# Kernel optimization log

Hardware: AMD Instinct MI355X
Metric: run time of the kernel (lower is better)

The kernel has to match this reference:

```python
import jax, jax.numpy as jnp
import numpy as np

E = 1024
H = 16
HD = E // H


def setup_inputs() -> dict:
    key = jax.random.key(0)
    k1, k2, k3, k4, k5 = jax.random.split(key, 5)
    x = jax.random.normal(k1, (2, 2048, E), dtype=jnp.float32)
    s = 1.0 / np.sqrt(E)
    qkv_w = jax.random.uniform(k2, (3 * E, E), jnp.float32, -s, s)
    qkv_b = jax.random.uniform(k3, (3 * E,), jnp.float32, -s, s)
    o_w = jax.random.uniform(k4, (E, E), jnp.float32, -s, s)
    o_b = jax.random.uniform(k5, (E,), jnp.float32, -s, s)
    return {"x": x, "qkv_w": qkv_w, "qkv_b": qkv_b, "o_w": o_w, "o_b": o_b}


def reference(x, qkv_w, qkv_b, o_w, o_b):
    B, T, _ = x.shape
    # qkv projection (torch Linear: x @ W.T + b)
    qkv = x @ qkv_w.T + qkv_b  # [B,T,3E]
    q, k, v = jnp.split(qkv, 3, axis=-1)
    # [B,H,T,HD]
    q = q.reshape(B, T, H, HD).transpose(0, 2, 1, 3)
    k = k.reshape(B, T, H, HD).transpose(0, 2, 1, 3)
    v = v.reshape(B, T, H, HD).transpose(0, 2, 1, 3)
    scores = jnp.einsum('bhqd,bhkd->bhqk', q, k) / np.sqrt(HD)
    causal = jnp.tril(jnp.ones((T, T), dtype=bool))
    scores = jnp.where(causal, scores, -jnp.inf)
    attn = jax.nn.softmax(scores, axis=-1)  # dropout disabled (eval mode)
    y = jnp.einsum('bhqk,bhkd->bhqd', attn, v)
    y = y.transpose(0, 2, 1, 3).reshape(B, T, E)
    return y @ o_w.T + o_b
```

## Files before the change

kernel.cpp:

```cpp
#include <hip/hip_runtime.h>
#include <hip/hip_bf16.h>
#include <math.h>

#define BATCH 2
#define SEQ   2048
#define EMB   1024
#define NH    16
#define HD    64
#define M_ROWS (BATCH * SEQ)

typedef __attribute__((ext_vector_type(8))) short bf16x8;
typedef __attribute__((ext_vector_type(4))) float f32x4;

__device__ __forceinline__ ushort f2bf(float f) {
    unsigned u = __float_as_uint(f);
    unsigned lsb = (u >> 16) & 1u;
    u += 0x7fffu + lsb;
    return (ushort)(u >> 16);
}

__device__ __forceinline__ unsigned cvt_pk_bf16(float lo, float hi) {
    unsigned r;
    asm("v_cvt_pk_bf16_f32 %0, %1, %2" : "=v"(r) : "v"(lo), "v"(hi));
    return r;
}

__device__ __forceinline__ void gload_lds16(const void* g, void* l) {
    __builtin_amdgcn_global_load_lds(
        (const __attribute__((address_space(1))) unsigned int*)g,
        (__attribute__((address_space(3))) unsigned int*)l, 16, 0, 0);
}

__global__ __launch_bounds__(256) void cvt3_f32_bf16(
    const float* __restrict__ s1, const float* __restrict__ s2,
    const float* __restrict__ s3, ushort* __restrict__ out,
    int n1, int n2)
{
    int i = (blockIdx.x * 256 + threadIdx.x) * 4;
    const float* src;
    int off;
    if (i < n1)            { src = s1; off = i; }
    else if (i < n1 + n2)  { src = s2; off = i - n1; }
    else                   { src = s3; off = i - n1 - n2; }
    float4 v = *reinterpret_cast<const float4*>(&src[off]);
    uint2 pk;
    pk.x = cvt_pk_bf16(v.x, v.y);
    pk.y = cvt_pk_bf16(v.z, v.w);
    *reinterpret_cast<uint2*>(&out[i]) = pk;
}

template <int MODE>
__global__ __launch_bounds__(256) void gemm_mfma_abt(
    const ushort* __restrict__ A, const ushort* __restrict__ B,
    const float* __restrict__ bias, float* __restrict__ Cout,
    ushort* __restrict__ qkb, ushort* __restrict__ vtb,
    int M, int N, int K)
{
    __shared__ ushort Al[128 * 64];
    __shared__ ushort Bl[128 * 64];

    const int tid  = threadIdx.x;
    const int lane = tid & 63;
    const int wave = tid >> 6;
    const int wr   = wave >> 1;
    const int wc   = wave & 1;
    const int l15  = lane & 15;
    const int l4   = lane >> 4;
    const int m0   = blockIdx.y * 128;
    const int n0   = blockIdx.x * 128;

    f32x4 acc[4][4];
#pragma unroll
    for (int m = 0; m < 4; ++m)
#pragma unroll
        for (int n = 0; n < 4; ++n)
#pragma unroll
            for (int r = 0; r < 4; ++r) acc[m][n][r] = 0.f;

    for (int k0 = 0; k0 < K; k0 += 64) {
#pragma unroll
        for (int it = 0; it < 4; ++it) {
            int chunk = tid + it * 256;
            int row = chunk >> 3;
            int kc  = (chunk & 7) * 8;
            gload_lds16(&A[(size_t)(m0 + row) * K + k0 + kc], &Al[chunk * 8]);
            gload_lds16(&B[(size_t)(n0 + row) * K + k0 + kc], &Bl[chunk * 8]);
        }
        __syncthreads();

#pragma unroll
        for (int kk = 0; kk < 2; ++kk) {
            const int ko = kk * 32 + l4 * 8;
            bf16x8 a[4], b[4];
#pragma unroll
            for (int m = 0; m < 4; ++m)
                a[m] = *reinterpret_cast<const bf16x8*>(
                    &Al[(wr * 64 + m * 16 + l15) * 64 + ko]);
#pragma unroll
            for (int n = 0; n < 4; ++n)
                b[n] = *reinterpret_cast<const bf16x8*>(
                    &Bl[(wc * 64 + n * 16 + l15) * 64 + ko]);
            __builtin_amdgcn_s_setprio(1);
#pragma unroll
            for (int m = 0; m < 4; ++m)
#pragma unroll
                for (int n = 0; n < 4; ++n)
                    acc[m][n] = __builtin_amdgcn_mfma_f32_16x16x32_bf16(
                        a[m], b[n], acc[m][n], 0, 0, 0);
            __builtin_amdgcn_s_setprio(0);
        }
        __syncthreads();
    }

#pragma unroll
    for (int n = 0; n < 4; ++n) {
        const int col = n0 + wc * 64 + n * 16 + l15;
        const float bv = bias[col];
        if (MODE == 0) {
#pragma unroll
            for (int m = 0; m < 4; ++m) {
                const int row0 = m0 + wr * 64 + m * 16 + l4 * 4;
#pragma unroll
                for (int r = 0; r < 4; ++r)
                    Cout[(size_t)(row0 + r) * N + col] = acc[m][n][r] + bv;
            }
        } else if (col < 2 * EMB) {
#pragma unroll
            for (int m = 0; m < 4; ++m) {
                const int row0 = m0 + wr * 64 + m * 16 + l4 * 4;
#pragma unroll
                for (int r = 0; r < 4; ++r)
                    qkb[(size_t)(row0 + r) * 2048 + col] = f2bf(acc[m][n][r] + bv);
            }
        } else {
            const int h = (col - 2 * EMB) >> 6;
            const int d = col & 63;
#pragma unroll
            for (int m = 0; m < 4; ++m) {
                const int row0 = m0 + wr * 64 + m * 16 + l4 * 4;
                const int bb = row0 >> 11;
                const int t  = row0 & 2047;
                uint2 pk;
                pk.x = cvt_pk_bf16(acc[m][n][0] + bv, acc[m][n][1] + bv);
                pk.y = cvt_pk_bf16(acc[m][n][2] + bv, acc[m][n][3] + bv);
                *reinterpret_cast<uint2*>(
                    &vtb[((size_t)(bb * 16 + h) * 64 + d) * 2048 + t]) = pk;
            }
        }
    }
}

__global__ __launch_bounds__(512) void attn_mfma(
    const ushort* __restrict__ qk, const ushort* __restrict__ vt,
    ushort* __restrict__ y)
{
    __shared__ alignas(16) ushort Kl[4][4096];
    __shared__ alignas(16) ushort Vl[4][4096];
    __shared__ alignas(16) ushort QP[8192];

    const int tid  = threadIdx.x;
    const int lane = tid & 63;
    const int w    = tid >> 6;
    const int l15  = lane & 15;
    const int l4   = lane >> 4;

    const int id  = blockIdx.x;
    const int xcd = id & 7;
    const int bh  = xcd * 4 + ((id >> 3) & 3);
    const int pp  = id >> 5;
    const int b   = bh >> 4;
    const int h   = bh & 15;

    const ushort* qbase = qk + (size_t)b * SEQ * 2048 + h * HD;
    const ushort* kbase = qbase + EMB;
    const ushort* vbase = vt + (size_t)bh * HD * SEQ;

    const int swz   = (l15 & 7) << 4;
    const int koff0 = ((l4 * 16) ^ swz) >> 1;
    const int koff1 = ((64 + l4 * 16) ^ swz) >> 1;

    int pso[4];
#pragma unroll
    for (int n = 0; n < 4; ++n) pso[n] = ((n * 32 + l4 * 8) ^ swz) >> 1;

    const short OBF = (short)0x3F80;
    const bf16x8 ones = {OBF, OBF, OBF, OBF, OBF, OBF, OBF, OBF};
    const float BETA = 0.18033688f;

    const int qrow = (w * 16 + l15) * 64;

    const int sr = tid >> 3;
    const int sc = ((tid & 7) ^ (sr & 7)) << 3;
    const int i2 = tid + 512;
    const int qr2 = i2 >> 3;
    const int qc2 = ((i2 & 7) ^ (qr2 & 7)) << 3;

#pragma unroll
    for (int pass = 0; pass < 2; ++pass) {
        const int qt  = pass ? (15 - pp) : pp;
        const int nkv = 2 * qt + 2;

        gload_lds16(qbase + (size_t)(qt * 128 + sr) * 2048 + sc, &QP[tid * 8]);
        gload_lds16(qbase + (size_t)(qt * 128 + qr2) * 2048 + qc2, &QP[i2 * 8]);
        gload_lds16(kbase + (size_t)sr * 2048 + sc, &Kl[0][tid * 8]);
        gload_lds16(kbase + (size_t)(64 + sr) * 2048 + sc, &Kl[1][tid * 8]);
        gload_lds16(vbase + (size_t)sr * 2048 + sc, &Vl[0][tid * 8]);
        gload_lds16(vbase + (size_t)sr * 2048 + 64 + sc, &Vl[1][tid * 8]);
        __syncthreads();

        const bf16x8 qf0 = *reinterpret_cast<const bf16x8*>(&QP[qrow + koff0]);
        const bf16x8 qf1 = *reinterpret_cast<const bf16x8*>(&QP[qrow + koff1]);

        f32x4 o[4];
#pragma unroll
        for (int n = 0; n < 4; ++n)
#pragma unroll
            for (int r = 0; r < 4; ++r) o[n][r] = 0.f;
        f32x4 lacc = {0.f, 0.f, 0.f, 0.f};
        float m = -3.0e38f;

        auto computeTile = [&](const ushort* Kb, const ushort* Vb, int kkt) {
            bf16x8 kf[4][2];
#pragma unroll
            for (int n = 0; n < 4; ++n) {
                kf[n][0] = *reinterpret_cast<const bf16x8*>(
                    &Kb[(n * 16 + l15) * 64 + koff0]);
                kf[n][1] = *reinterpret_cast<const bf16x8*>(
                    &Kb[(n * 16 + l15) * 64 + koff1]);
            }
            f32x4 s[4];
            __builtin_amdgcn_s_setprio(1);
#pragma unroll
            for (int n = 0; n < 4; ++n) {
                f32x4 z = {0.f, 0.f, 0.f, 0.f};
                z = __builtin_amdgcn_mfma_f32_16x16x32_bf16(kf[n][0], qf0, z, 0, 0, 0);
                s[n] = __builtin_amdgcn_mfma_f32_16x16x32_bf16(kf[n][1], qf1, z, 0, 0, 0);
            }
            __builtin_amdgcn_s_setprio(0);

            bf16x8 vf[4][2];
#pragma unroll
            for (int n = 0; n < 4; ++n) {
                vf[n][0] = *reinterpret_cast<const bf16x8*>(
                    &Vb[(n * 16 + l15) * 64 + koff0]);
                vf[n][1] = *reinterpret_cast<const bf16x8*>(
                    &Vb[(n * 16 + l15) * 64 + koff1]);
            }

            if (kkt >= nkv - 2) {
                const int q0 = qt * 128 + w * 16 + l15;
#pragma unroll
                for (int n = 0; n < 4; ++n)
#pragma unroll
                    for (int r = 0; r < 4; ++r) {
                        int kg = kkt * 64 + n * 16 + l4 * 4 + r;
                        if (kg > q0) s[n][r] = -3.0e38f;
                    }
            }

            float a0 = fmaxf(fmaxf(s[0][0], s[0][1]), fmaxf(s[0][2], s[0][3]));
            float a1 = fmaxf(fmaxf(s[1][0], s[1][1]), fmaxf(s[1][2], s[1][3]));
            float a2 = fmaxf(fmaxf(s[2][0], s[2][1]), fmaxf(s[2][2], s[2][3]));
            float a3 = fmaxf(fmaxf(s[3][0], s[3][1]), fmaxf(s[3][2], s[3][3]));
            float pm = fmaxf(fmaxf(a0, a1), fmaxf(a2, a3)) * BETA;

            if (__any(pm > m + 8.0f)) {
                float tm = fmaxf(pm, __shfl_xor(pm, 16));
                tm = fmaxf(tm, __shfl_xor(tm, 32));
                float mn = fmaxf(m, tm);
                float al = exp2f(m - mn);
                m = mn;
                float b0 = __shfl(al, l4 * 4 + 0, 16);
                float b1 = __shfl(al, l4 * 4 + 1, 16);
                float b2 = __shfl(al, l4 * 4 + 2, 16);
                float b3 = __shfl(al, l4 * 4 + 3, 16);
                lacc[0] *= b0; lacc[1] *= b1; lacc[2] *= b2; lacc[3] *= b3;
#pragma unroll
                for (int n = 0; n < 4; ++n) {
                    o[n][0] *= b0; o[n][1] *= b1; o[n][2] *= b2; o[n][3] *= b3;
                }
            }

#pragma unroll
            for (int n = 0; n < 4; ++n) {
                float pa = exp2f(fmaf(s[n][0], BETA, -m));
                float pb = exp2f(fmaf(s[n][1], BETA, -m));
                float pc = exp2f(fmaf(s[n][2], BETA, -m));
                float pd = exp2f(fmaf(s[n][3], BETA, -m));
                uint2 pk;
                pk.x = cvt_pk_bf16(pa, pb);
                pk.y = cvt_pk_bf16(pc, pd);
                *reinterpret_cast<uint2*>(&QP[qrow + pso[n]]) = pk;
            }

            bf16x8 pf0 = *reinterpret_cast<const bf16x8*>(&QP[qrow + koff0]);
            bf16x8 pf1 = *reinterpret_cast<const bf16x8*>(&QP[qrow + koff1]);
            __builtin_amdgcn_s_setprio(1);
            lacc = __builtin_amdgcn_mfma_f32_16x16x32_bf16(pf0, ones, lacc, 0, 0, 0);
            lacc = __builtin_amdgcn_mfma_f32_16x16x32_bf16(pf1, ones, lacc, 0, 0, 0);
#pragma unroll
            for (int n = 0; n < 4; ++n) {
                o[n] = __builtin_amdgcn_mfma_f32_16x16x32_bf16(pf0, vf[n][0], o[n], 0, 0, 0);
                o[n] = __builtin_amdgcn_mfma_f32_16x16x32_bf16(pf1, vf[n][1], o[n], 0, 0, 0);
            }
            __builtin_amdgcn_s_setprio(0);
        };

        for (int kk = 0; kk < nkv; kk += 2) {
            if (kk + 2 < nkv) {
                const int b2 = (kk + 2) & 3;
                const int b3 = (kk + 3) & 3;
                gload_lds16(kbase + (size_t)((kk + 2) * 64 + sr) * 2048 + sc,
                            &Kl[b2][tid * 8]);
                gload_lds16(kbase + (size_t)((kk + 3) * 64 + sr) * 2048 + sc,
                            &Kl[b3][tid * 8]);
                gload_lds16(vbase + (size_t)sr * 2048 + (kk + 2) * 64 + sc,
                            &Vl[b2][tid * 8]);
                gload_lds16(vbase + (size_t)sr * 2048 + (kk + 3) * 64 + sc,
                            &Vl[b3][tid * 8]);
            }
            computeTile(Kl[kk & 3], Vl[kk & 3], kk);
            computeTile(Kl[(kk + 1) & 3], Vl[(kk + 1) & 3], kk + 1);
            __syncthreads();
        }

#pragma unroll
        for (int r = 0; r < 4; ++r) {
            float inv = 1.f / lacc[r];
            int row = qt * 128 + w * 16 + l4 * 4 + r;
#pragma unroll
            for (int n = 0; n < 4; ++n) {
                y[(size_t)(b * SEQ + row) * EMB + h * HD + n * 16 + l15] =
                    f2bf(o[n][r] * inv);
            }
        }
        __syncthreads();
    }
}

extern "C" void kernel_launch(void* const* d_in, const int* in_sizes, int n_in,
                              void* d_out, int out_size, void* d_ws, size_t ws_size,
                              hipStream_t stream)
{
    const float* x     = (const float*)d_in[0];
    const float* qkv_w = (const float*)d_in[1];
    const float* qkv_b = (const float*)d_in[2];
    const float* o_w   = (const float*)d_in[3];
    const float* o_b   = (const float*)d_in[4];
    float* out = (float*)d_out;

    ushort* xb    = (ushort*)d_ws;
    ushort* wqkvb = xb    + (size_t)M_ROWS * EMB;
    ushort* owb   = wqkvb + (size_t)3 * EMB * EMB;
    ushort* qkb   = owb   + (size_t)EMB * EMB;
    ushort* vtb   = qkb   + (size_t)M_ROWS * 2 * EMB;
    ushort* ybb   = vtb   + (size_t)32 * HD * SEQ;

    {
        int n1 = M_ROWS * EMB;
        int n2 = 3 * EMB * EMB;
        int ntot = n1 + n2 + EMB * EMB;
        cvt3_f32_bf16<<<ntot / 1024, 256, 0, stream>>>(
            x, qkv_w, o_w, xb, n1, n2);
    }

    {
        dim3 grid(3 * EMB / 128, M_ROWS / 128);
        gemm_mfma_abt<1><<<grid, 256, 0, stream>>>(
            xb, wqkvb, qkv_b, nullptr, qkb, vtb, M_ROWS, 3 * EMB, EMB);
    }

    {
        attn_mfma<<<256, 512, 0, stream>>>(qkb, vtb, ybb);
    }

    {
        dim3 grid(EMB / 128, M_ROWS / 128);
        gemm_mfma_abt<0><<<grid, 256, 0, stream>>>(
            ybb, owb, o_b, out, nullptr, nullptr, M_ROWS, EMB, EMB);
    }
}
```

Measured before the change: 113.7 us.

## Stage QKV GEMM epilogue through LDS, fold softmax scale into Q, skip masked tiles

The QKV GEMM epilogue now writes bf16 results into a swizzled LDS tile and then emits coalesced 16-byte global stores for both the Q/K buffer and the transposed V buffer, replacing scattered 2-byte and 8-byte stores. The softmax scale (log2e/sqrt(d)) is multiplied into Q in the GEMM epilogue, which removes the per-element multiply in the attention kernel's exp path. In the last KV tile pair, waves 0-3 skip the second tile because it is fully masked for their query rows. This adds an LDS round trip and a barrier to the GEMM epilogue, and rounding Q to bf16 after scaling slightly changes numerics.

```diff
diff --git a/kernel.cpp b/kernel.cpp
--- a/kernel.cpp
+++ b/kernel.cpp
@@ -56,8 +56,10 @@
     ushort* __restrict__ qkb, ushort* __restrict__ vtb,
     int M, int N, int K)
 {
-    __shared__ ushort Al[128 * 64];
-    __shared__ ushort Bl[128 * 64];
+    __shared__ ushort LDSbuf[128 * 128];
+    ushort* Al = LDSbuf;
+    ushort* Bl = LDSbuf + 128 * 64;
+    ushort* CT = LDSbuf;
 
     const int tid  = threadIdx.x;
     const int lane = tid & 63;
@@ -112,11 +114,11 @@
         __syncthreads();
     }
 
-#pragma unroll
-    for (int n = 0; n < 4; ++n) {
-        const int col = n0 + wc * 64 + n * 16 + l15;
-        const float bv = bias[col];
-        if (MODE == 0) {
+    if (MODE == 0) {
+#pragma unroll
+        for (int n = 0; n < 4; ++n) {
+            const int col = n0 + wc * 64 + n * 16 + l15;
+            const float bv = bias[col];
 #pragma unroll
             for (int m = 0; m < 4; ++m) {
                 const int row0 = m0 + wr * 64 + m * 16 + l4 * 4;
@@ -124,28 +126,65 @@
                 for (int r = 0; r < 4; ++r)
                     Cout[(size_t)(row0 + r) * N + col] = acc[m][n][r] + bv;
             }
-        } else if (col < 2 * EMB) {
+        }
+    } else if (n0 < 2 * EMB) {
+#pragma unroll
+        for (int n = 0; n < 4; ++n) {
+            const int Cc = wc * 64 + n * 16 + l15;
+            const int colg = n0 + Cc;
+            const float bv = bias[colg];
+            const float qs = (colg < EMB) ? 0.18033688f : 1.0f;
 #pragma unroll
             for (int m = 0; m < 4; ++m) {
-                const int row0 = m0 + wr * 64 + m * 16 + l4 * 4;
-#pragma unroll
-                for (int r = 0; r < 4; ++r)
-                    qkb[(size_t)(row0 + r) * 2048 + col] = f2bf(acc[m][n][r] + bv);
-            }
-        } else {
-            const int h = (col - 2 * EMB) >> 6;
-            const int d = col & 63;
+#pragma unroll
+                for (int r = 0; r < 4; ++r) {
+                    int R = wr * 64 + m * 16 + l4 * 4 + r;
+                    CT[R * 128 + (Cc ^ ((R & 7) << 3))] =
+                        f2bf((acc[m][n][r] + bv) * qs);
+                }
+            }
+        }
+        __syncthreads();
+#pragma unroll
+        for (int j = 0; j < 8; ++j) {
+            int f  = tid + j * 256;
+            int R  = f >> 4;
+            int c0 = (f & 15) * 8;
+            uint4 v = *reinterpret_cast<const uint4*>(
+                &CT[R * 128 + (c0 ^ ((R & 7) << 3))]);
+            *reinterpret_cast<uint4*>(
+                &qkb[(size_t)(m0 + R) * 2048 + n0 + c0]) = v;
+        }
+    } else {
+#pragma unroll
+        for (int n = 0; n < 4; ++n) {
+            const int Cc = wc * 64 + n * 16 + l15;
+            const float bv = bias[n0 + Cc];
 #pragma unroll
             for (int m = 0; m < 4; ++m) {
-                const int row0 = m0 + wr * 64 + m * 16 + l4 * 4;
-                const int bb = row0 >> 11;
-                const int t  = row0 & 2047;
-                uint2 pk;
-                pk.x = cvt_pk_bf16(acc[m][n][0] + bv, acc[m][n][1] + bv);
-                pk.y = cvt_pk_bf16(acc[m][n][2] + bv, acc[m][n][3] + bv);
-                *reinterpret_cast<uint2*>(
-                    &vtb[((size_t)(bb * 16 + h) * 64 + d) * 2048 + t]) = pk;
-            }
+#pragma unroll
+                for (int r = 0; r < 4; ++r) {
+                    int R = wr * 64 + m * 16 + l4 * 4 + r;
+                    CT[Cc * 128 + (R ^ ((Cc & 7) << 3))] =
+                        f2bf(acc[m][n][r] + bv);
+                }
+            }
+        }
+        __syncthreads();
+        const int bb = m0 >> 11;
+        const int tb = m0 & 2047;
+#pragma unroll
+        for (int j = 0; j < 8; ++j) {
+            int f  = tid + j * 256;
+            int D  = f >> 4;
+            int t0 = (f & 15) * 8;
+            uint4 v = *reinterpret_cast<const uint4*>(
+                &CT[D * 128 + (t0 ^ ((D & 7) << 3))]);
+            int dg = (n0 - 2 * EMB) + D;
+            int h  = dg >> 6;
+            int dd = dg & 63;
+            *reinterpret_cast<uint4*>(
+                &vtb[((size_t)(bb * 16 + h) * 64 + dd) * 2048 + tb + t0]) = v;
         }
     }
 }
@@ -185,7 +224,6 @@
 
     const short OBF = (short)0x3F80;
     const bf16x8 ones = {OBF, OBF, OBF, OBF, OBF, OBF, OBF, OBF};
-    const float BETA = 0.18033688f;
 
     const int qrow = (w * 16 + l15) * 64;
 
@@ -219,6 +257,8 @@
         f32x4 lacc = {0.f, 0.f, 0.f, 0.f};
         float m = -3.0e38f;
 
+        const int q0g = qt * 128 + w * 16 + l15;
+
         auto computeTile = [&](const ushort* Kb, const ushort* Vb, int kkt) {
             bf16x8 kf[4][2];
 #pragma unroll
@@ -248,13 +288,12 @@
             }
 
             if (kkt >= nkv - 2) {
-                const int q0 = qt * 128 + w * 16 + l15;
 #pragma unroll
                 for (int n = 0; n < 4; ++n)
 #pragma unroll
                     for (int r = 0; r < 4; ++r) {
                         int kg = kkt * 64 + n * 16 + l4 * 4 + r;
-                        if (kg > q0) s[n][r] = -3.0e38f;
+                        if (kg > q0g) s[n][r] = -3.0e38f;
                     }
             }
 
@@ -262,7 +301,7 @@
             float a1 = fmaxf(fmaxf(s[1][0], s[1][1]), fmaxf(s[1][2], s[1][3]));
             float a2 = fmaxf(fmaxf(s[2][0], s[2][1]), fmaxf(s[2][2], s[2][3]));
             float a3 = fmaxf(fmaxf(s[3][0], s[3][1]), fmaxf(s[3][2], s[3][3]));
-            float pm = fmaxf(fmaxf(a0, a1), fmaxf(a2, a3)) * BETA;
+            float pm = fmaxf(fmaxf(a0, a1), fmaxf(a2, a3));
 
             if (__any(pm > m + 8.0f)) {
                 float tm = fmaxf(pm, __shfl_xor(pm, 16));
@@ -283,10 +322,10 @@
 
 #pragma unroll
             for (int n = 0; n < 4; ++n) {
-                float pa = exp2f(fmaf(s[n][0], BETA, -m));
-                float pb = exp2f(fmaf(s[n][1], BETA, -m));
-                float pc = exp2f(fmaf(s[n][2], BETA, -m));
-                float pd = exp2f(fmaf(s[n][3], BETA, -m));
+                float pa = exp2f(s[n][0] - m);
+                float pb = exp2f(s[n][1] - m);
+                float pc = exp2f(s[n][2] - m);
+                float pd = exp2f(s[n][3] - m);
                 uint2 pk;
                 pk.x = cvt_pk_bf16(pa, pb);
                 pk.y = cvt_pk_bf16(pc, pd);
@@ -320,7 +359,8 @@
                             &Vl[b3][tid * 8]);
             }
             computeTile(Kl[kk & 3], Vl[kk & 3], kk);
-            computeTile(Kl[(kk + 1) & 3], Vl[(kk + 1) & 3], kk + 1);
+            if (!(kk == nkv - 2 && w < 4))
+                computeTile(Kl[(kk + 1) & 3], Vl[(kk + 1) & 3], kk + 1);
             __syncthreads();
         }
 
```

After: 127.9 us. 1.13x slower.
